# Kernel tuning notes

Hardware: AMD Instinct MI355X
Metric: run time of the kernel (lower is better)

Reference implementation:

```python
import jax, jax.numpy as jnp
import numpy as np

N = 50000
NEG_SLOPE = 0.2  # PyG GATConv default negative_slope


def gat_conv(x, src, dst, W, a_src, a_dst, b, num_nodes):
    """PyG-style GATConv (concat=True, add_self_loops handled by caller).
    x: [N, Fin], src/dst: [E'] (self-loops included), W: [Fin, H*C],
    a_src/a_dst: [H, C], b: [H*C].
    """
    H, C = a_src.shape
    h = (x @ W).reshape(num_nodes, H, C)                      # [N, H, C]
    alpha_src = jnp.einsum('nhc,hc->nh', h, a_src)            # [N, H]
    alpha_dst = jnp.einsum('nhc,hc->nh', h, a_dst)            # [N, H]
    e = jax.nn.leaky_relu(alpha_src[src] + alpha_dst[dst], NEG_SLOPE)  # [E', H]
    # segment softmax over edges grouped by destination node
    m = jax.ops.segment_max(e, dst, num_segments=num_nodes)   # [N, H]
    m = jnp.where(jnp.isfinite(m), m, 0.0)
    ex = jnp.exp(e - m[dst])                                  # [E', H]
    denom = jax.ops.segment_sum(ex, dst, num_segments=num_nodes)
    alpha = ex / (denom[dst] + 1e-16)                          # [E', H]
    # weighted scatter-sum of source features to destinations
    out = jax.ops.segment_sum(alpha[:, :, None] * h[src], dst, num_segments=num_nodes)
    return out.reshape(num_nodes, H * C) + b


def setup_inputs() -> dict:
    key = jax.random.key(0)
    ks = jax.random.split(key, 10)
    Fin, Hid, Out, Hds = 128, 32, 64, 4
    E = 800000
    x = jax.random.normal(ks[0], (N, Fin), dtype=jnp.float32)
    edge_index = jax.random.randint(ks[1], (2, E), 0, N, dtype=jnp.int64)
    s1 = (1.0 / np.sqrt(Fin)).astype(np.float32) if isinstance(np.sqrt(Fin), np.ndarray) else np.float32(1.0 / np.sqrt(Fin))
    s2 = np.float32(1.0 / np.sqrt(Hid * Hds))
    return {
        'x': x,
        'edge_index': edge_index,
        'W1': jax.random.normal(ks[2], (Fin, Hds * Hid), dtype=jnp.float32) * s1,
        'att_src1': jax.random.normal(ks[3], (Hds, Hid), dtype=jnp.float32) * 0.1,
        'att_dst1': jax.random.normal(ks[4], (Hds, Hid), dtype=jnp.float32) * 0.1,
        'b1': jnp.zeros((Hds * Hid,), dtype=jnp.float32),
        'W2': jax.random.normal(ks[5], (Hds * Hid, Out), dtype=jnp.float32) * s2,
        'att_src2': jax.random.normal(ks[6], (1, Out), dtype=jnp.float32) * 0.1,
        'att_dst2': jax.random.normal(ks[7], (1, Out), dtype=jnp.float32) * 0.1,
        'b2': jnp.zeros((Out,), dtype=jnp.float32),
    }


def reference(x, edge_index, W1, att_src1, att_dst1, b1, W2, att_src2, att_dst2, b2):
    num_nodes = x.shape[0]
    loop = jnp.arange(num_nodes, dtype=edge_index.dtype)
    src = jnp.concatenate([edge_index[0], loop])  # add self-loops (PyG default)
    dst = jnp.concatenate([edge_index[1], loop])
    h = gat_conv(x, src, dst, W1, att_src1, att_dst1, b1, num_nodes)
    h = jax.nn.relu(h)
    out = gat_conv(h, src, dst, W2, att_src2, att_dst2, b2, num_nodes)
    return out
```

## Files before the change

kernel.cpp:

```cpp
#include <hip/hip_runtime.h>
#include <hip/hip_fp16.h>

#define NN 50000
#define EE 800000
#define ELL (EE + NN)
#define NSLICE 8
#define SLICE_W (NN / NSLICE)
#define LCAP 131072
#define LCNT_STRIDE 16
#define BUCK_TILE 4096

__device__ __forceinline__ int edge_at(const void* ei, int is64, long long idx) {
  if (is64) return (int)((const long long*)ei)[idx];
  return ((const int*)ei)[idx];
}

__device__ __forceinline__ float leaky(float x) { return x > 0.f ? x : 0.2f * x; }


__global__ void __launch_bounds__(256) zero_detect_kernel(int* __restrict__ p, int n,
                                                          const unsigned* __restrict__ ei_words,
                                                          int* __restrict__ flag) {
  if (blockIdx.x == 0 && threadIdx.x == 0) {
    unsigned acc = 0;
    for (int i = 1; i < 64; i += 2) acc |= ei_words[i];
    *flag = (acc == 0u) ? 1 : 0;
  }
  int stride = gridDim.x * blockDim.x;
  for (int i = blockIdx.x * blockDim.x + threadIdx.x; i < n; i += stride) p[i] = 0;
}


__global__ void __launch_bounds__(256) bucket_kernel(const void* __restrict__ ei,
                                                     const int* __restrict__ flag,
                                                     unsigned* __restrict__ lists,
                                                     int* __restrict__ lcnt) {
  __shared__ int hist[NSLICE];
  __shared__ int base[NSLICE];
  __shared__ int cur[NSLICE];
  int is64 = *flag;
  int t = threadIdx.x;
  if (t < NSLICE) hist[t] = 0;
  __syncthreads();
  long long i0 = (long long)blockIdx.x * BUCK_TILE;
  unsigned pk[16];
  int sl[16];
  #pragma unroll
  for (int j = 0; j < 16; ++j) {
    long long i = i0 + t + j * 256;
    int s = -1, d = -1;
    if (i < EE) {
      s = edge_at(ei, is64, i);
      d = edge_at(ei, is64, (long long)EE + i);
    } else if (i < ELL) {
      s = d = (int)(i - EE);
    }
    if ((unsigned)s < (unsigned)NN && (unsigned)d < (unsigned)NN) {
      sl[j] = d / SLICE_W;
      pk[j] = (unsigned)s | ((unsigned)d << 16);
      atomicAdd(&hist[sl[j]], 1);
    } else {
      sl[j] = -1;
    }
  }
  __syncthreads();
  if (t < NSLICE) {
    base[t] = atomicAdd(&lcnt[t * LCNT_STRIDE], hist[t]);
    cur[t] = 0;
  }
  __syncthreads();
  #pragma unroll
  for (int j = 0; j < 16; ++j) {
    if (sl[j] >= 0) {
      int pos = base[sl[j]] + atomicAdd(&cur[sl[j]], 1);
      if (pos < LCAP) lists[(sl[j] << 17) + pos] = pk[j];
    }
  }
}


__global__ void __launch_bounds__(256) count_kernel(const unsigned* __restrict__ lists,
                                                    const int* __restrict__ lcnt,
                                                    int* __restrict__ cnt) {
  int fam = blockIdx.x & (NSLICE - 1);
  int bf = blockIdx.x >> 3;
  int nf = gridDim.x >> 3;
  int n = min(lcnt[fam * LCNT_STRIDE], LCAP);
  const unsigned* lp = lists + (fam << 17);
  for (int i = bf * blockDim.x + threadIdx.x; i < n; i += nf * blockDim.x)
    atomicAdd(&cnt[lp[i] >> 16], 1);
}

__global__ void __launch_bounds__(256) scan1_kernel(const int* __restrict__ cnt,
                                                    int* __restrict__ excl,
                                                    int* __restrict__ bsum) {
  __shared__ int sh[256];
  int t = threadIdx.x;
  int base = blockIdx.x * 1024 + t * 4;
  int v0 = 0, v1 = 0, v2 = 0, v3 = 0;
  if (base + 0 < NN) v0 = cnt[base + 0];
  if (base + 1 < NN) v1 = cnt[base + 1];
  if (base + 2 < NN) v2 = cnt[base + 2];
  if (base + 3 < NN) v3 = cnt[base + 3];
  int s = v0 + v1 + v2 + v3;
  sh[t] = s;
  __syncthreads();
  for (int off = 1; off < 256; off <<= 1) {
    int x = (t >= off) ? sh[t - off] : 0;
    __syncthreads();
    sh[t] += x;
    __syncthreads();
  }
  if (t == 255) bsum[blockIdx.x] = sh[255];
  int run = sh[t] - s;
  if (base + 0 < NN) excl[base + 0] = run;
  run += v0;
  if (base + 1 < NN) excl[base + 1] = run;
  run += v1;
  if (base + 2 < NN) excl[base + 2] = run;
  run += v2;
  if (base + 3 < NN) excl[base + 3] = run;
}

__global__ void scan2_kernel(int* __restrict__ bsum, int nb) {
  if (threadIdx.x == 0 && blockIdx.x == 0) {
    int run = 0;
    for (int i = 0; i < nb; ++i) { int x = bsum[i]; bsum[i] = run; run += x; }
    bsum[nb] = run;
  }
}

__global__ void __launch_bounds__(256) scan3_kernel(int* __restrict__ row_ptr,
                                                    const int* __restrict__ bsum,
                                                    int nb) {
  int i = blockIdx.x * blockDim.x + threadIdx.x;
  if (i < NN) row_ptr[i] += bsum[i >> 10];
  if (i == 0) row_ptr[NN] = bsum[nb];
}

__global__ void __launch_bounds__(256) scatter_kernel(const unsigned* __restrict__ lists,
                                                      const int* __restrict__ lcnt,
                                                      const int* __restrict__ row_ptr,
                                                      int* __restrict__ cursor,
                                                      unsigned* __restrict__ pairs) {
  int fam = blockIdx.x & (NSLICE - 1);
  int bf = blockIdx.x >> 3;
  int nf = gridDim.x >> 3;
  int n = min(lcnt[fam * LCNT_STRIDE], LCAP);
  const unsigned* lp = lists + (fam << 17);
  for (int i = bf * blockDim.x + threadIdx.x; i < n; i += nf * blockDim.x) {
    unsigned pk = lp[i];
    int d = pk >> 16;
    int pos = row_ptr[d] + atomicAdd(&cursor[d], 1);
    if ((unsigned)pos < (unsigned)ELL) pairs[pos] = pk;
  }
}

__global__ void __launch_bounds__(256) weight1_kernel(const unsigned* __restrict__ pairs,
                                                      const float* __restrict__ asrc,
                                                      const float* __restrict__ adst,
                                                      __half* __restrict__ w1h) {
  int stride = gridDim.x * blockDim.x;
  for (int i = blockIdx.x * blockDim.x + threadIdx.x; i < ELL; i += stride) {
    unsigned pk = pairs[i];
    int s = pk & 0xFFFF, d = pk >> 16;
    float4 as4 = *(const float4*)&asrc[s * 4];
    float4 ad4 = *(const float4*)&adst[d * 4];
    __half hw[4];
    hw[0] = __float2half(__expf(leaky(as4.x + ad4.x)));
    hw[1] = __float2half(__expf(leaky(as4.y + ad4.y)));
    hw[2] = __float2half(__expf(leaky(as4.z + ad4.z)));
    hw[3] = __float2half(__expf(leaky(as4.w + ad4.w)));
    *(uint2*)&w1h[(size_t)i * 4] = *(uint2*)hw;
  }
}


template <int BM, int BN, int BK, int TM, int TN, int AMODE>
__global__ void __launch_bounds__(256) gemm_alpha(const float* __restrict__ A,
                                                  const float* __restrict__ B,
                                                  __half* __restrict__ C,
                                                  const float* __restrict__ a_srcv,
                                                  const float* __restrict__ a_dstv,
                                                  float* __restrict__ asrc_out,
                                                  float* __restrict__ adst_out,
                                                  int M, int N, int K) {
  constexpr int THREADS = (BM / TM) * (BN / TN);
  static_assert(THREADS == 256, "block must be 256 threads");
  static_assert(BM * BK == 1024, "A tile = 4 floats/thread");
  static_assert((TN % 4) == 0 && (TM % 4) == 0, "microtile shape");
  constexpr int BPT = (BK * BN) / THREADS;
  static_assert(BPT == 2 || BPT == 4, "B tile load width");
  __shared__ float As[BK][BM + 4];
  __shared__ float Bs[BK][BN + 4];
  int tid = threadIdx.x;
  int tx = tid % (BN / TN);
  int ty = tid / (BN / TN);
  int row0 = blockIdx.x * BM;
  int col0 = blockIdx.y * BN;
  float acc[TM][TN] = {};
  for (int k0 = 0; k0 < K; k0 += BK) {
    {
      int m = tid / (BK / 4);
      int kk = (tid % (BK / 4)) * 4;
      float4 v = make_float4(0.f, 0.f, 0.f, 0.f);
      int gr = row0 + m;
      if (gr < M) v = *(const float4*)&A[(size_t)gr * K + k0 + kk];
      As[kk + 0][m] = v.x; As[kk + 1][m] = v.y;
      As[kk + 2][m] = v.z; As[kk + 3][m] = v.w;
    }
    if constexpr (BPT == 4) {
      constexpr int T_PER_ROW = BN / 4;
      int kr = tid / T_PER_ROW;
      int nc = (tid % T_PER_ROW) * 4;
      *(float4*)&Bs[kr][nc] = *(const float4*)&B[(size_t)(k0 + kr) * N + col0 + nc];
    } else {
      constexpr int T_PER_ROW = BN / 2;
      int kr = tid / T_PER_ROW;
      int nc = (tid % T_PER_ROW) * 2;
      *(float2*)&Bs[kr][nc] = *(const float2*)&B[(size_t)(k0 + kr) * N + col0 + nc];
    }
    __syncthreads();
    #pragma unroll
    for (int k = 0; k < BK; ++k) {
      float a[TM], b[TN];
      #pragma unroll
      for (int i = 0; i < TM; i += 4)
        *(float4*)&a[i] = *(const float4*)&As[k][ty * TM + i];
      #pragma unroll
      for (int j = 0; j < TN; j += 4)
        *(float4*)&b[j] = *(const float4*)&Bs[k][tx * TN + j];
      #pragma unroll
      for (int i = 0; i < TM; ++i)
        #pragma unroll
        for (int j = 0; j < TN; ++j) acc[i][j] += a[i] * b[j];
    }
    __syncthreads();
  }
  #pragma unroll
  for (int i = 0; i < TM; ++i) {
    int gr = row0 + ty * TM + i;
    if (gr >= M) continue;
    __half tmp[TN];
    #pragma unroll
    for (int j = 0; j < TN; ++j) tmp[j] = __float2half(acc[i][j]);
    if constexpr (TN == 8)
      *(float4*)&C[(size_t)gr * N + col0 + tx * TN] = *(float4*)tmp;
    else
      *(float2*)&C[(size_t)gr * N + col0 + tx * TN] = *(float2*)tmp;
  }
  if (AMODE == 1) {
    int hh = tx >> 2;
    int co = (tx & 3) * TN;
    #pragma unroll
    for (int i = 0; i < TM; ++i) {
      float sA = 0.f, sD = 0.f;
      #pragma unroll
      for (int j = 0; j < TN; ++j) {
        float v = acc[i][j];
        sA += v * a_srcv[hh * 32 + co + j];
        sD += v * a_dstv[hh * 32 + co + j];
      }
      sA += __shfl_xor(sA, 1, 64); sA += __shfl_xor(sA, 2, 64);
      sD += __shfl_xor(sD, 1, 64); sD += __shfl_xor(sD, 2, 64);
      int gr = row0 + ty * TM + i;
      if ((tx & 3) == 0 && gr < M) {
        asrc_out[gr * 4 + hh] = sA;
        adst_out[gr * 4 + hh] = sD;
      }
    }
  } else if (AMODE == 2) {
    #pragma unroll
    for (int i = 0; i < TM; ++i) {
      float sA = 0.f, sD = 0.f;
      #pragma unroll
      for (int j = 0; j < TN; ++j) {
        float v = acc[i][j];
        sA += v * a_srcv[tx * TN + j];
        sD += v * a_dstv[tx * TN + j];
      }
      #pragma unroll
      for (int m = 1; m <= 8; m <<= 1) {
        sA += __shfl_xor(sA, m, 64);
        sD += __shfl_xor(sD, m, 64);
      }
      int gr = row0 + ty * TM + i;
      if (tx == 0 && gr < M) { asrc_out[gr] = sA; adst_out[gr] = sD; }
    }
  }
}


__global__ void __launch_bounds__(256) agg1_fused(
    const __half* __restrict__ h,
    const int* __restrict__ row_ptr,
    const unsigned* __restrict__ pairs,
    const __half* __restrict__ w1h,
    const float* __restrict__ b1,
    float* __restrict__ out)
{
  int lane = threadIdx.x & 63;
  int grp = lane >> 5;
  int cl = lane & 31;
  int c0 = cl * 4;
  int myh = cl >> 3;
  int wid = (blockIdx.x * blockDim.x + threadIdx.x) >> 6;
  int nw = (gridDim.x * blockDim.x) >> 6;
  float4 bb = *(const float4*)&b1[c0];
  for (int n = wid; n < NN; n += nw) {
    int rbeg = row_ptr[n], rend = row_ptr[n + 1];
    float dsum = grp ? 0.f : 1e-16f;
    float a0 = 0.f, a1 = 0.f, a2 = 0.f, a3 = 0.f;
    #pragma unroll 4
    for (int e = rbeg + grp; e < rend; e += 2) {
      int s = pairs[e] & 0xFFFF;
      uint2 wraw = *(const uint2*)&w1h[(size_t)e * 4];
      unsigned wsel = (myh & 2) ? wraw.y : wraw.x;
      __half2 hw = __builtin_bit_cast(__half2, wsel);
      float wgt = (myh & 1) ? __high2float(hw) : __low2float(hw);
      float2 raw = *(const float2*)&h[(size_t)s * 128 + c0];
      float2 f01 = __half22float2(__builtin_bit_cast(__half2, raw.x));
      float2 f23 = __half22float2(__builtin_bit_cast(__half2, raw.y));
      dsum += wgt;
      a0 += wgt * f01.x; a1 += wgt * f01.y;
      a2 += wgt * f23.x; a3 += wgt * f23.y;
    }
    dsum += __shfl_xor(dsum, 32, 64);
    a0 += __shfl_xor(a0, 32, 64);
    a1 += __shfl_xor(a1, 32, 64);
    a2 += __shfl_xor(a2, 32, 64);
    a3 += __shfl_xor(a3, 32, 64);
    if (lane < 32) {
      float inv = 1.f / dsum;
      float4 o = make_float4(fmaxf(a0 * inv + bb.x, 0.f),
                             fmaxf(a1 * inv + bb.y, 0.f),
                             fmaxf(a2 * inv + bb.z, 0.f),
                             fmaxf(a3 * inv + bb.w, 0.f));
      *(float4*)&out[(size_t)n * 128 + c0] = o;
    }
  }
}

__global__ void __launch_bounds__(256) agg2_kernel(
    const __half* __restrict__ h,
    const int* __restrict__ row_ptr,
    const unsigned* __restrict__ pairs,
    const float* __restrict__ asrc,
    const float* __restrict__ adst,
    const float* __restrict__ b2,
    float* __restrict__ out)
{
  int lane = threadIdx.x & 63;
  int grp = lane >> 4;
  int cl = lane & 15;
  int c0 = cl * 4;
  int wid = (blockIdx.x * blockDim.x + threadIdx.x) >> 6;
  int nw = (gridDim.x * blockDim.x) >> 6;
  float4 bb = *(const float4*)&b2[c0];
  for (int n = wid; n < NN; n += nw) {
    int rbeg = row_ptr[n], rend = row_ptr[n + 1];
    float ad = adst[n];
    float dsum = (grp == 0) ? 1e-16f : 0.f;
    float a0 = 0.f, a1 = 0.f, a2 = 0.f, a3 = 0.f;
    #pragma unroll 4
    for (int e = rbeg + grp; e < rend; e += 4) {
      int s = pairs[e] & 0xFFFF;
      float wgt = __expf(leaky(asrc[s] + ad));
      float2 raw = *(const float2*)&h[(size_t)s * 64 + c0];
      float2 f01 = __half22float2(__builtin_bit_cast(__half2, raw.x));
      float2 f23 = __half22float2(__builtin_bit_cast(__half2, raw.y));
      dsum += wgt;
      a0 += wgt * f01.x; a1 += wgt * f01.y;
      a2 += wgt * f23.x; a3 += wgt * f23.y;
    }
    #pragma unroll
    for (int m = 16; m <= 32; m <<= 1) {
      dsum += __shfl_xor(dsum, m, 64);
      a0 += __shfl_xor(a0, m, 64);
      a1 += __shfl_xor(a1, m, 64);
      a2 += __shfl_xor(a2, m, 64);
      a3 += __shfl_xor(a3, m, 64);
    }
    if (lane < 16) {
      float inv = 1.f / dsum;
      float4 o = make_float4(a0 * inv + bb.x, a1 * inv + bb.y,
                             a2 * inv + bb.z, a3 * inv + bb.w);
      *(float4*)&out[(size_t)n * 64 + c0] = o;
    }
  }
}


extern "C" void kernel_launch(void* const* d_in, const int* in_sizes, int n_in,
                              void* d_out, int out_size, void* d_ws, size_t ws_size,
                              hipStream_t stream) {
  const float* x   = (const float*)d_in[0];
  const void*  ei  = d_in[1];
  const float* W1  = (const float*)d_in[2];
  const float* as1 = (const float*)d_in[3];
  const float* ad1 = (const float*)d_in[4];
  const float* b1  = (const float*)d_in[5];
  const float* W2  = (const float*)d_in[6];
  const float* as2 = (const float*)d_in[7];
  const float* ad2 = (const float*)d_in[8];
  const float* b2  = (const float*)d_in[9];
  float* out = (float*)d_out;

  char* w = (char*)d_ws;
  __half* h1h  = (__half*)w; w += (size_t)NN * 128 * 2;
  __half* hb2h = h1h;
  float* h2    = (float*)w; w += (size_t)NN * 128 * 4;
  float* asrc1 = (float*)w; w += (size_t)NN * 4 * 4;
  float* adst1 = (float*)w; w += (size_t)NN * 4 * 4;
  float* asrc2 = (float*)w; w += (size_t)NN * 4;
  float* adst2 = (float*)w; w += (size_t)NN * 4;
  int* cnt     = (int*)w;   w += (size_t)NN * 4;
  int* cursor  = (int*)w;   w += (size_t)NN * 4;
  int* lcnt    = (int*)w;   w += 512;
  int* row_ptr = (int*)w;   w += (size_t)(NN + 1) * 4;
  int* bsum    = (int*)w;   w += 256;
  int* is64    = (int*)w;   w += 256;
  unsigned* lists = (unsigned*)w; w += (size_t)NSLICE * LCAP * 4;
  unsigned* pairs = (unsigned*)w; w += (size_t)ELL * 4;
  __half* w1h  = (__half*)w; w += (size_t)ELL * 4 * 2;

  const int NB = (NN + 1023) / 1024;
  const int MB128 = (NN + 127) / 128;
  const int BUCK_BLOCKS = (ELL + BUCK_TILE - 1) / BUCK_TILE;

  zero_detect_kernel<<<256, 256, 0, stream>>>(cnt, 2 * NN + 128, (const unsigned*)ei, is64);
  bucket_kernel<<<BUCK_BLOCKS, 256, 0, stream>>>(ei, is64, lists, lcnt);
  count_kernel<<<2048, 256, 0, stream>>>(lists, lcnt, cnt);
  scan1_kernel<<<NB, 256, 0, stream>>>(cnt, row_ptr, bsum);
  scan2_kernel<<<1, 64, 0, stream>>>(bsum, NB);
  scan3_kernel<<<(NN + 255) / 256, 256, 0, stream>>>(row_ptr, bsum, NB);

  gemm_alpha<128, 128, 8, 8, 8, 1><<<dim3(MB128, 1), 256, 0, stream>>>(
      x, W1, h1h, as1, ad1, asrc1, adst1, NN, 128, 128);

  scatter_kernel<<<2048, 256, 0, stream>>>(lists, lcnt, row_ptr, cursor, pairs);
  weight1_kernel<<<2048, 256, 0, stream>>>(pairs, asrc1, adst1, w1h);

  agg1_fused<<<4096, 256, 0, stream>>>(h1h, row_ptr, pairs, w1h, b1, h2);

  gemm_alpha<128, 64, 8, 8, 4, 2><<<dim3(MB128, 1), 256, 0, stream>>>(
      h2, W2, hb2h, as2, ad2, asrc2, adst2, NN, 64, 128);
  agg2_kernel<<<4096, 256, 0, stream>>>(hb2h, row_ptr, pairs, asrc2, adst2, b2, out);
}
```

Before: 227.3 us.

## Fuse attention weight computation into layer-1 aggregation and store hidden in fp16

Removes the separate weight1 kernel that precomputed per-edge exp weights into an fp16 buffer. Instead, each lane recomputes its head's weight inline inside agg1 from asrc/adst gathers, with a deeper unroll. The layer-1 output is now written as fp16, and the second GEMM is templated to read half-precision A. This cuts a kernel launch plus the edge-weight write and read, and halves the h2 traffic. The cost is redundant exp and gather work per lane and extra fp16 rounding of the hidden features.

```diff
diff --git a/kernel.cpp b/kernel.cpp
--- a/kernel.cpp
+++ b/kernel.cpp
@@ -156,28 +156,9 @@
   }
 }
 
-__global__ void __launch_bounds__(256) weight1_kernel(const unsigned* __restrict__ pairs,
-                                                      const float* __restrict__ asrc,
-                                                      const float* __restrict__ adst,
-                                                      __half* __restrict__ w1h) {
-  int stride = gridDim.x * blockDim.x;
-  for (int i = blockIdx.x * blockDim.x + threadIdx.x; i < ELL; i += stride) {
-    unsigned pk = pairs[i];
-    int s = pk & 0xFFFF, d = pk >> 16;
-    float4 as4 = *(const float4*)&asrc[s * 4];
-    float4 ad4 = *(const float4*)&adst[d * 4];
-    __half hw[4];
-    hw[0] = __float2half(__expf(leaky(as4.x + ad4.x)));
-    hw[1] = __float2half(__expf(leaky(as4.y + ad4.y)));
-    hw[2] = __float2half(__expf(leaky(as4.z + ad4.z)));
-    hw[3] = __float2half(__expf(leaky(as4.w + ad4.w)));
-    *(uint2*)&w1h[(size_t)i * 4] = *(uint2*)hw;
-  }
-}
-
-
-template <int BM, int BN, int BK, int TM, int TN, int AMODE>
-__global__ void __launch_bounds__(256) gemm_alpha(const float* __restrict__ A,
+
+template <typename TA, int BM, int BN, int BK, int TM, int TN, int AMODE>
+__global__ void __launch_bounds__(256) gemm_alpha(const TA* __restrict__ A,
                                                   const float* __restrict__ B,
                                                   __half* __restrict__ C,
                                                   const float* __restrict__ a_srcv,
@@ -187,7 +168,7 @@
                                                   int M, int N, int K) {
   constexpr int THREADS = (BM / TM) * (BN / TN);
   static_assert(THREADS == 256, "block must be 256 threads");
-  static_assert(BM * BK == 1024, "A tile = 4 floats/thread");
+  static_assert(BM * BK == 1024, "A tile = 4 elems/thread");
   static_assert((TN % 4) == 0 && (TM % 4) == 0, "microtile shape");
   constexpr int BPT = (BK * BN) / THREADS;
   static_assert(BPT == 2 || BPT == 4, "B tile load width");
@@ -203,11 +184,21 @@
     {
       int m = tid / (BK / 4);
       int kk = (tid % (BK / 4)) * 4;
-      float4 v = make_float4(0.f, 0.f, 0.f, 0.f);
       int gr = row0 + m;
-      if (gr < M) v = *(const float4*)&A[(size_t)gr * K + k0 + kk];
-      As[kk + 0][m] = v.x; As[kk + 1][m] = v.y;
-      As[kk + 2][m] = v.z; As[kk + 3][m] = v.w;
+      float va[4] = {0.f, 0.f, 0.f, 0.f};
+      if (gr < M) {
+        if constexpr (sizeof(TA) == 4) {
+          float4 v = *(const float4*)&A[(size_t)gr * K + k0 + kk];
+          va[0] = v.x; va[1] = v.y; va[2] = v.z; va[3] = v.w;
+        } else {
+          uint2 raw = *(const uint2*)&A[(size_t)gr * K + k0 + kk];
+          float2 f01 = __half22float2(__builtin_bit_cast(__half2, raw.x));
+          float2 f23 = __half22float2(__builtin_bit_cast(__half2, raw.y));
+          va[0] = f01.x; va[1] = f01.y; va[2] = f23.x; va[3] = f23.y;
+        }
+      }
+      As[kk + 0][m] = va[0]; As[kk + 1][m] = va[1];
+      As[kk + 2][m] = va[2]; As[kk + 3][m] = va[3];
     }
     if constexpr (BPT == 4) {
       constexpr int T_PER_ROW = BN / 4;
@@ -295,9 +286,10 @@
     const __half* __restrict__ h,
     const int* __restrict__ row_ptr,
     const unsigned* __restrict__ pairs,
-    const __half* __restrict__ w1h,
+    const float* __restrict__ asrc,
+    const float* __restrict__ adst,
     const float* __restrict__ b1,
-    float* __restrict__ out)
+    __half* __restrict__ out)
 {
   int lane = threadIdx.x & 63;
   int grp = lane >> 5;
@@ -309,15 +301,13 @@
   float4 bb = *(const float4*)&b1[c0];
   for (int n = wid; n < NN; n += nw) {
     int rbeg = row_ptr[n], rend = row_ptr[n + 1];
+    float ad = adst[n * 4 + myh];
     float dsum = grp ? 0.f : 1e-16f;
     float a0 = 0.f, a1 = 0.f, a2 = 0.f, a3 = 0.f;
-    #pragma unroll 4
+    #pragma unroll 8
     for (int e = rbeg + grp; e < rend; e += 2) {
       int s = pairs[e] & 0xFFFF;
-      uint2 wraw = *(const uint2*)&w1h[(size_t)e * 4];
-      unsigned wsel = (myh & 2) ? wraw.y : wraw.x;
-      __half2 hw = __builtin_bit_cast(__half2, wsel);
-      float wgt = (myh & 1) ? __high2float(hw) : __low2float(hw);
+      float wgt = __expf(leaky(asrc[s * 4 + myh] + ad));
       float2 raw = *(const float2*)&h[(size_t)s * 128 + c0];
       float2 f01 = __half22float2(__builtin_bit_cast(__half2, raw.x));
       float2 f23 = __half22float2(__builtin_bit_cast(__half2, raw.y));
@@ -332,11 +322,12 @@
     a3 += __shfl_xor(a3, 32, 64);
     if (lane < 32) {
       float inv = 1.f / dsum;
-      float4 o = make_float4(fmaxf(a0 * inv + bb.x, 0.f),
-                             fmaxf(a1 * inv + bb.y, 0.f),
-                             fmaxf(a2 * inv + bb.z, 0.f),
-                             fmaxf(a3 * inv + bb.w, 0.f));
-      *(float4*)&out[(size_t)n * 128 + c0] = o;
+      __half ot[4];
+      ot[0] = __float2half(fmaxf(a0 * inv + bb.x, 0.f));
+      ot[1] = __float2half(fmaxf(a1 * inv + bb.y, 0.f));
+      ot[2] = __float2half(fmaxf(a2 * inv + bb.z, 0.f));
+      ot[3] = __float2half(fmaxf(a3 * inv + bb.w, 0.f));
+      *(uint2*)&out[(size_t)n * 128 + c0] = *(uint2*)ot;
     }
   }
 }
@@ -409,7 +400,7 @@
   char* w = (char*)d_ws;
   __half* h1h  = (__half*)w; w += (size_t)NN * 128 * 2;
   __half* hb2h = h1h;
-  float* h2    = (float*)w; w += (size_t)NN * 128 * 4;
+  __half* h2   = (__half*)w; w += (size_t)NN * 128 * 2;
   float* asrc1 = (float*)w; w += (size_t)NN * 4 * 4;
   float* adst1 = (float*)w; w += (size_t)NN * 4 * 4;
   float* asrc2 = (float*)w; w += (size_t)NN * 4;
@@ -422,7 +413,6 @@
   int* is64    = (int*)w;   w += 256;
   unsigned* lists = (unsigned*)w; w += (size_t)NSLICE * LCAP * 4;
   unsigned* pairs = (unsigned*)w; w += (size_t)ELL * 4;
-  __half* w1h  = (__half*)w; w += (size_t)ELL * 4 * 2;
 
   const int NB = (NN + 1023) / 1024;
   const int MB128 = (NN + 127) / 128;
@@ -435,15 +425,14 @@
   scan2_kernel<<<1, 64, 0, stream>>>(bsum, NB);
   scan3_kernel<<<(NN + 255) / 256, 256, 0, stream>>>(row_ptr, bsum, NB);
 
-  gemm_alpha<128, 128, 8, 8, 8, 1><<<dim3(MB128, 1), 256, 0, stream>>>(
+  gemm_alpha<float, 128, 128, 8, 8, 8, 1><<<dim3(MB128, 1), 256, 0, stream>>>(
       x, W1, h1h, as1, ad1, asrc1, adst1, NN, 128, 128);
 
   scatter_kernel<<<2048, 256, 0, stream>>>(lists, lcnt, row_ptr, cursor, pairs);
-  weight1_kernel<<<2048, 256, 0, stream>>>(pairs, asrc1, adst1, w1h);
-
-  agg1_fused<<<4096, 256, 0, stream>>>(h1h, row_ptr, pairs, w1h, b1, h2);
-
-  gemm_alpha<128, 64, 8, 8, 4, 2><<<dim3(MB128, 1), 256, 0, stream>>>(
+
+  agg1_fused<<<4096, 256, 0, stream>>>(h1h, row_ptr, pairs, asrc1, adst1, b1, h2);
+
+  gemm_alpha<__half, 128, 64, 8, 8, 4, 2><<<dim3(MB128, 1), 256, 0, stream>>>(
       h2, W2, hb2h, as2, ad2, asrc2, adst2, NN, 64, 128);
   agg2_kernel<<<4096, 256, 0, stream>>>(hb2h, row_ptr, pairs, asrc2, adst2, b2, out);
 }
```

Result: no change. 231.2 us (+1.7%).
